# Performance work log

Hardware: AMD Instinct MI355X
Metric: run time of the kernel (lower is better)

The kernel has to match this reference:

```python
import jax, jax.numpy as jnp
import numpy as np

H = 56; W = 56; WS = 7; SHIFT = 3; C = 256; NH = 8
HD = C // NH; N = WS * WS; NW = (H // WS) * (W // WS)
SCALE = HD ** -0.5
LN_EPS = 1e-5


def _rel_pos_index():
    coords = np.stack(np.meshgrid(np.arange(WS), np.arange(WS), indexing='ij'))  # (2, ws, ws)
    cf = coords.reshape(2, -1)
    rel = (cf[:, :, None] - cf[:, None, :]).transpose(1, 2, 0)  # (N, N, 2)
    rel[..., 0] += WS - 1
    rel[..., 1] += WS - 1
    rel[..., 0] *= 2 * WS - 1
    return rel.sum(-1)  # (N, N) indices into (2*ws-1)^2 table

RPI = jnp.asarray(_rel_pos_index())


def _attn_mask():
    img = np.zeros((H, W))
    slices = (slice(0, -WS), slice(-WS, -SHIFT), slice(-SHIFT, None))
    cnt = 0
    for hs in slices:
        for ws_ in slices:
            img[hs, ws_] = cnt
            cnt += 1
    mw = img.reshape(H // WS, WS, W // WS, WS).transpose(0, 2, 1, 3).reshape(-1, N)
    diff = mw[:, None, :] - mw[:, :, None]  # (nW, N, N), [w,i,j] = mw[w,j]-mw[w,i]
    return jnp.asarray(np.where(diff != 0, -100.0, 0.0).astype(np.float32))

AMASK = _attn_mask()  # (nW, N, N)


def ln(x, g, b):
    m = x.mean(-1, keepdims=True)
    v = x.var(-1, keepdims=True)
    return (x - m) / jnp.sqrt(v + LN_EPS) * g + b


def win_part(x):  # (B, H, W, C) -> (B*nW, N, C)
    B = x.shape[0]
    return x.reshape(B, H // WS, WS, W // WS, WS, C).transpose(0, 1, 3, 2, 4, 5).reshape(-1, N, C)


def win_rev(xw, B):  # (B*nW, N, C) -> (B, H, W, C)
    return xw.reshape(B, H // WS, W // WS, WS, WS, C).transpose(0, 1, 3, 2, 4, 5).reshape(B, H, W, C)


def setup_inputs() -> dict:
    key = jax.random.key(0)
    ks = iter(jax.random.split(key, 40))
    B, L = 16, H * W
    Ch = int(C * 4.0)
    p = {}
    p['x'] = jax.random.normal(next(ks), (B, L, C), jnp.float32)
    p['x_SAR'] = jax.random.normal(next(ks), (B, L, C), jnp.float32)
    p['ln1_g'] = jnp.ones((C,)); p['ln1_b'] = jnp.zeros((C,))
    p['ln1s_g'] = jnp.ones((C,)); p['ln1s_b'] = jnp.zeros((C,))
    p['qkv_w'] = jax.random.normal(next(ks), (3 * C, C)) * 0.02
    p['qkv_b'] = jnp.zeros((3 * C,))
    p['qkvs_w'] = jax.random.normal(next(ks), (3 * C, C)) * 0.02
    p['qkvs_b'] = jnp.zeros((3 * C,))
    p['rpb_table'] = jax.random.normal(next(ks), ((2 * WS - 1) ** 2, NH)) * 0.02
    p['fuse_w'] = jax.random.normal(next(ks), (NH, NH)) * 0.1  # Conv2d(8,8,1) weight squeezed
    p['fuse_b'] = jnp.zeros((NH,))
    p['proj_w'] = jax.random.normal(next(ks), (C, C)) * 0.02
    p['proj_b'] = jnp.zeros((C,))
    p['projs_w'] = jax.random.normal(next(ks), (C, C)) * 0.02
    p['projs_b'] = jnp.zeros((C,))
    p['ln2_g'] = jnp.ones((C,)); p['ln2_b'] = jnp.zeros((C,))
    p['ln2s_g'] = jnp.ones((C,)); p['ln2s_b'] = jnp.zeros((C,))
    p['fc1_w'] = jax.random.normal(next(ks), (Ch, C)) * 0.02
    p['fc1_b'] = jnp.zeros((Ch,))
    p['fc2_w'] = jax.random.normal(next(ks), (C, Ch)) * 0.02
    p['fc2_b'] = jnp.zeros((C,))
    p['fc1s_w'] = jax.random.normal(next(ks), (Ch, C)) * 0.02
    p['fc1s_b'] = jnp.zeros((Ch,))
    p['fc2s_w'] = jax.random.normal(next(ks), (C, Ch)) * 0.02
    p['fc2s_b'] = jnp.zeros((C,))
    return p


def reference(x, x_SAR, ln1_g, ln1_b, ln1s_g, ln1s_b, qkv_w, qkv_b, qkvs_w, qkvs_b,
              rpb_table, fuse_w, fuse_b, proj_w, proj_b, projs_w, projs_b,
              ln2_g, ln2_b, ln2s_g, ln2s_b, fc1_w, fc1_b, fc2_w, fc2_b,
              fc1s_w, fc1s_b, fc2s_w, fc2s_b):
    B = x.shape[0]
    sc, sc_s = x, x_SAR

    def pre(xx, g, b):  # norm -> spatial -> cyclic shift -> windows
        xs = ln(xx, g, b).reshape(B, H, W, C)
        xs = jnp.roll(xs, (-SHIFT, -SHIFT), axis=(1, 2))
        return win_part(xs)

    xw = pre(x, ln1_g, ln1_b)
    xws = pre(x_SAR, ln1s_g, ln1s_b)

    def qkv_f(xin, Wt, bt):
        qkv = (xin @ Wt.T + bt).reshape(-1, N, 3, NH, HD).transpose(2, 0, 3, 1, 4)
        return qkv[0], qkv[1], qkv[2]  # each (B*nW, nH, N, HD)

    q, k, v = qkv_f(xw, qkv_w, qkv_b)
    qs, ks_, vs = qkv_f(xws, qkvs_w, qkvs_b)

    attn = jnp.einsum('bhnd,bhmd->bhnm', q * SCALE, k)
    attn_s = jnp.einsum('bhnd,bhmd->bhnm', qs * SCALE, ks_)

    rpb = rpb_table[RPI.reshape(-1)].reshape(N, N, NH).transpose(2, 0, 1)  # (nH, N, N)
    attn = attn + rpb[None]
    attn_s = attn_s + rpb[None]

    # shift-window mask add
    attn = (attn.reshape(B, NW, NH, N, N) + AMASK[None, :, None]).reshape(-1, NH, N, N)
    attn_s = (attn_s.reshape(B, NW, NH, N, N) + AMASK[None, :, None]).reshape(-1, NH, N, N)

    # dual-branch fusion: 1x1 conv over head dim + sigmoid gate
    diff = attn_s - attn
    gate = jax.nn.sigmoid(jnp.einsum('oh,bhnm->bonm', fuse_w, diff) + fuse_b[None, :, None, None])
    attn_f = jax.nn.softmax(attn + diff * gate, axis=-1)
    attn_s = jax.nn.softmax(attn_s, axis=-1)

    def out_f(a, vv, pw, pb):
        o = jnp.einsum('bhnm,bhmd->bhnd', a, vv).transpose(0, 2, 1, 3).reshape(-1, N, C)
        return o @ pw.T + pb

    xo = out_f(attn_f, v, proj_w, proj_b)
    xos = out_f(attn_s, vs, projs_w, projs_b)

    def post(xout, scc, g2, b2, w1, b1, w2, b2m):
        xr = jnp.roll(win_rev(xout, B), (SHIFT, SHIFT), axis=(1, 2)).reshape(B, -1, C)
        xr = scc + xr
        h = jax.nn.gelu(ln(xr, g2, b2) @ w1.T + b1, approximate=False)
        return xr + (h @ w2.T + b2m)

    out = post(xo, sc, ln2_g, ln2_b, fc1_w, fc1_b, fc2_w, fc2_b)
    out_s = post(xos, sc_s, ln2s_g, ln2s_b, fc1s_w, fc1s_b, fc2s_w, fc2s_b)
    return out, out_s
```

## Files before the change

kernel.cpp:

```cpp
#include <hip/hip_runtime.h>
#include <hip/hip_bf16.h>
#include <cstdio>

typedef unsigned short ushort_t;
using bf16x8  = __attribute__((ext_vector_type(8))) __bf16;
using u16x8   = __attribute__((ext_vector_type(8))) unsigned short;
using floatx4 = __attribute__((ext_vector_type(4))) float;

constexpr int    kTokens = 50176;
constexpr size_t TCsz    = (size_t)kTokens * 256;
constexpr float  kScale  = 0.17677669529663687f;
constexpr int    PSTR    = 904;
constexpr size_t VTP     = 2048;
constexpr size_t VTSZ    = (size_t)8192 * VTP;

__device__ __forceinline__ float bf2f(ushort_t u) {
  unsigned int x = (unsigned int)u << 16;
  return __uint_as_float(x);
}
__device__ __forceinline__ ushort_t f2bf(float f) {
  __hip_bfloat16 h = __float2bfloat16(f);
  return *(ushort_t*)&h;
}

__device__ __forceinline__ void gl_lds16(const ushort_t* g, ushort_t* l) {
  __builtin_amdgcn_global_load_lds(
      (const __attribute__((address_space(1))) unsigned int*)g,
      (__attribute__((address_space(3))) unsigned int*)l, 16, 0, 0);
}

__global__ __launch_bounds__(256) void f2b_k(const float* __restrict__ src,
                                             ushort_t* __restrict__ dst, int n) {
  int i = blockIdx.x * 256 + threadIdx.x;
  if (i < n) dst[i] = f2bf(src[i]);
}

__global__ __launch_bounds__(64) void bias2_k(const float* __restrict__ rpb,
                                              float* __restrict__ biasf) {
  const int b = blockIdx.x;
  const int head = b & 7, chunk = (b >> 3) & 3, cls = b >> 5;
  const int wh7 = cls >> 1, ww7 = cls & 1;
  const int lane = threadIdx.x;
  float* bp = biasf + ((size_t)b * 64 + lane) * 16;
#pragma unroll
  for (int nt = 0; nt < 4; ++nt) {
#pragma unroll
    for (int r = 0; r < 4; ++r) {
      const int row = chunk * 16 + (lane >> 4) * 4 + r;
      const int col = nt * 16 + (lane & 15);
      float val = 0.0f;
      if (row < 49 && col < 49) {
        const int yi = row / 7, xi = row % 7, yj = col / 7, xj = col % 7;
        val = rpb[((yi - yj + 6) * 13 + (xi - xj + 6)) * 8 + head];
        const int li = (wh7 ? (yi < 4 ? 1 : 2) : 0) * 3 + (ww7 ? (xi < 4 ? 1 : 2) : 0);
        const int lj = (wh7 ? (yj < 4 ? 1 : 2) : 0) * 3 + (ww7 ? (xj < 4 ? 1 : 2) : 0);
        if (li != lj) val -= 100.0f;
      }
      bp[nt * 4 + r] = val;
    }
  }
}

__global__ __launch_bounds__(256) void vtz_k(ushort_t* __restrict__ vtA,
                                             ushort_t* __restrict__ vtB) {
  const int id = blockIdx.x * 256 + threadIdx.x;
  ushort_t* base = (id < 262144) ? vtA : vtB;
  const size_t r = (size_t)(id & 262143) * 64;
  const uint4 z{0, 0, 0, 0};
  *(uint4*)(base + r + 48) = z;
  *(uint4*)(base + r + 56) = z;
}

template <int SHIFTED>
__global__ __launch_bounds__(256) void ln_k(const float* __restrict__ x,
                                            const float* __restrict__ g,
                                            const float* __restrict__ b,
                                            ushort_t* __restrict__ yout) {
  const int wave = threadIdx.x >> 6, lane = threadIdx.x & 63;
  const int t = blockIdx.x * 4 + wave;
  size_t src;
  if (SHIFTED) {
    int bb = t / 3136, r = t % 3136;
    int wi = r / 49, n = r % 49;
    int hp = (wi >> 3) * 7 + n / 7;
    int wp = (wi & 7) * 7 + n % 7;
    int sh = hp + 3; if (sh >= 56) sh -= 56;
    int sw = wp + 3; if (sw >= 56) sw -= 56;
    src = ((size_t)bb * 3136 + sh * 56 + sw) * 256;
  } else {
    src = (size_t)t * 256;
  }
  const float4 v4 = *(const float4*)(x + src + lane * 4);
  float s  = v4.x + v4.y + v4.z + v4.w;
  float s2 = v4.x * v4.x + v4.y * v4.y + v4.z * v4.z + v4.w * v4.w;
#pragma unroll
  for (int off = 32; off > 0; off >>= 1) {
    s  += __shfl_xor(s,  off);
    s2 += __shfl_xor(s2, off);
  }
  const float mean = s * (1.0f / 256.0f);
  const float var  = s2 * (1.0f / 256.0f) - mean * mean;
  const float rstd = rsqrtf(var + 1e-5f);
  const float4 g4 = *(const float4*)(g + lane * 4);
  const float4 b4 = *(const float4*)(b + lane * 4);
  ushort4 o;
  o.x = f2bf((v4.x - mean) * rstd * g4.x + b4.x);
  o.y = f2bf((v4.y - mean) * rstd * g4.y + b4.y);
  o.z = f2bf((v4.z - mean) * rstd * g4.z + b4.z);
  o.w = f2bf((v4.w - mean) * rstd * g4.w + b4.w);
  *(ushort4*)(yout + (size_t)t * 256 + lane * 4) = o;
}

template <int MODE>
__global__ __launch_bounds__(256) void bgemm_k(const ushort_t* __restrict__ A,
                                               const ushort_t* __restrict__ W,
                                               const float* __restrict__ bias,
                                               float* __restrict__ outf,
                                               ushort_t* __restrict__ outb,
                                               const float* __restrict__ aux,
                                               int K, int Nc) {
  __shared__ __align__(16) ushort_t As[2 * 4096];
  __shared__ __align__(16) ushort_t Bs[2 * 4096];
  const int tid = threadIdx.x;
  const int nbx = gridDim.x;
  const int nwg = nbx * gridDim.y;
  int flat = blockIdx.y * nbx + blockIdx.x;
  {
    const int xcd = flat & 7, idx = flat >> 3;
    const int q8 = nwg >> 3, r8 = nwg & 7;
    flat = (xcd < r8 ? xcd * (q8 + 1) : r8 * (q8 + 1) + (xcd - r8) * q8) + idx;
  }
  const int m0 = (flat / nbx) * 128;
  const int n0 = (flat % nbx) * 128;
  const int lane = tid & 63, wv = tid >> 6;
  const int wm = (wv >> 1) * 64, wn = (wv & 1) * 64;
  const int l16 = lane & 15, quad = lane >> 4;

  const int srow = tid >> 2;
  const int gkc  = (tid & 3) ^ ((tid >> 3) & 3);
  const ushort_t* Ag0 = A + (size_t)(m0 + srow) * K + gkc * 8;
  const ushort_t* Ag1 = A + (size_t)(m0 + 64 + srow) * K + gkc * 8;
  const ushort_t* Wg0 = W + (size_t)(n0 + srow) * K + gkc * 8;
  const ushort_t* Wg1 = W + (size_t)(n0 + 64 + srow) * K + gkc * 8;
  const int ldsW0 = wv * 512, ldsW1 = 2048 + wv * 512;

  const int kcq = quad ^ ((l16 >> 1) & 3);
  const int arA = (wm + l16) * 32 + kcq * 8;
  const int arB = (wn + l16) * 32 + kcq * 8;

  const int NT = K >> 5;
  floatx4 acc[4][4] = {};

  gl_lds16(Ag0, As + ldsW0);
  gl_lds16(Ag1, As + ldsW1);
  gl_lds16(Wg0, Bs + ldsW0);
  gl_lds16(Wg1, Bs + ldsW1);
  __syncthreads();

  int cur = 0;
  for (int t = 0; t < NT; ++t) {
    if (t + 1 < NT) {
      const int k0 = (t + 1) * 32;
      const int nb = (cur ^ 1) * 4096;
      gl_lds16(Ag0 + k0, As + nb + ldsW0);
      gl_lds16(Ag1 + k0, As + nb + ldsW1);
      gl_lds16(Wg0 + k0, Bs + nb + ldsW0);
      gl_lds16(Wg1 + k0, Bs + nb + ldsW1);
    }
    const int cb = cur * 4096;
    bf16x8 af[4], bfr[4];
#pragma unroll
    for (int tt = 0; tt < 4; ++tt) {
      af[tt]  = *(const bf16x8*)&As[cb + arA + tt * 512];
      bfr[tt] = *(const bf16x8*)&Bs[cb + arB + tt * 512];
    }
#pragma unroll
    for (int mt = 0; mt < 4; ++mt)
#pragma unroll
      for (int nt = 0; nt < 4; ++nt)
        acc[mt][nt] = __builtin_amdgcn_mfma_f32_16x16x32_bf16(af[mt], bfr[nt], acc[mt][nt], 0, 0, 0);
    __syncthreads();
    cur ^= 1;
  }

  if (MODE == 0) {
    int wis[16], ns[16];
#pragma unroll
    for (int mt = 0; mt < 4; ++mt) {
      int row = m0 + wm + mt * 16 + quad * 4;
      int wi = row / 49, n = row - wi * 49;
#pragma unroll
      for (int r = 0; r < 4; ++r) {
        wis[mt * 4 + r] = wi; ns[mt * 4 + r] = n;
        if (++n == 49) { n = 0; ++wi; }
      }
    }
    if (n0 < 512) {
      size_t rb[16];
#pragma unroll
      for (int i = 0; i < 16; ++i) rb[i] = (size_t)wis[i] * 12544 + (size_t)ns[i] * 32;
#pragma unroll
      for (int nt = 0; nt < 4; ++nt) {
        const int col = n0 + wn + nt * 16 + l16;
        const int which = col >> 8, head = (col >> 5) & 7, d = col & 31;
        const float bv = bias[col];
        const float sc = (which == 0) ? kScale : 1.0f;
        ushort_t* ob = outb + (size_t)which * TCsz + head * 1568 + d;
#pragma unroll
        for (int i = 0; i < 16; ++i)
          ob[rb[i]] = f2bf((acc[i >> 2][nt][i & 3] + bv) * sc);
      }
    } else {
      size_t rb[16];
#pragma unroll
      for (int i = 0; i < 16; ++i) rb[i] = (size_t)wis[i] * 16384 + (size_t)ns[i];
      ushort_t* vtb = (ushort_t*)outf;
#pragma unroll
      for (int nt = 0; nt < 4; ++nt) {
        const int col = n0 + wn + nt * 16 + l16;
        const int head = (col >> 5) & 7, d = col & 31;
        const float bv = bias[col];
        ushort_t* ob = vtb + head * 2048 + d * 64;
#pragma unroll
        for (int i = 0; i < 16; ++i)
          ob[rb[i]] = f2bf(acc[i >> 2][nt][i & 3] + bv);
      }
    }
  } else if (MODE == 1) {
    size_t rb[16];
#pragma unroll
    for (int mt = 0; mt < 4; ++mt) {
#pragma unroll
      for (int r = 0; r < 4; ++r) {
        const int row = m0 + wm + mt * 16 + quad * 4 + r;
        const int wi = row / 49, n = row - wi * 49;
        const int b = wi >> 6, wl = wi & 63;
        int h = (wl >> 3) * 7 + n / 7 + 3; if (h >= 56) h -= 56;
        int w = (wl & 7) * 7 + n % 7 + 3; if (w >= 56) w -= 56;
        rb[mt * 4 + r] = ((size_t)(b * 3136 + h * 56 + w)) * 256;
      }
    }
#pragma unroll
    for (int nt = 0; nt < 4; ++nt) {
      const int col = n0 + wn + nt * 16 + l16;
      const float bv = bias[col];
#pragma unroll
      for (int i = 0; i < 16; ++i) {
        const size_t idx = rb[i] + col;
        outf[idx] = aux[idx] + acc[i >> 2][nt][i & 3] + bv;
      }
    }
  } else if (MODE == 2) {
    size_t rb[16];
#pragma unroll
    for (int mt = 0; mt < 4; ++mt)
#pragma unroll
      for (int r = 0; r < 4; ++r)
        rb[mt * 4 + r] = (size_t)(m0 + wm + mt * 16 + quad * 4 + r) * Nc;
#pragma unroll
    for (int nt = 0; nt < 4; ++nt) {
      const int col = n0 + wn + nt * 16 + l16;
      const float bv = bias[col];
#pragma unroll
      for (int i = 0; i < 16; ++i) {
        float val = acc[i >> 2][nt][i & 3] + bv;
        val = 0.5f * val * (1.0f + erff(val * 0.70710678118654752f));
        outb[rb[i] + col] = f2bf(val);
      }
    }
  } else {
    size_t rb[16];
#pragma unroll
    for (int mt = 0; mt < 4; ++mt)
#pragma unroll
      for (int r = 0; r < 4; ++r)
        rb[mt * 4 + r] = (size_t)(m0 + wm + mt * 16 + quad * 4 + r) * 256;
#pragma unroll
    for (int nt = 0; nt < 4; ++nt) {
      const int col = n0 + wn + nt * 16 + l16;
      const float bv = bias[col];
#pragma unroll
      for (int i = 0; i < 16; ++i) {
        const size_t idx = rb[i] + col;
        outf[idx] = aux[idx] + acc[i >> 2][nt][i & 3] + bv;
      }
    }
  }
}

__global__ __launch_bounds__(256) void attn_k(const ushort_t* __restrict__ qA,
                                              const ushort_t* __restrict__ qB,
                                              const ushort_t* __restrict__ vtA,
                                              const ushort_t* __restrict__ vtB,
                                              const float* __restrict__ biasf,
                                              const float* __restrict__ fw,
                                              const float* __restrict__ fb,
                                              ushort_t* __restrict__ Obase) {
  __shared__ __align__(16) ushort_t S[16 * PSTR];
  __shared__ float fwl[64], fbl[8];
  __shared__ float linv[256];
  const int tid = threadIdx.x, lane = tid & 63, wv = tid >> 6;
  const int l16 = lane & 15, quad = lane >> 4;
  int bx = blockIdx.x;
  bx = (bx & 7) * 512 + (bx >> 3);
  const int win = bx >> 2, chunk = bx & 3;
  const int r0 = chunk * 16;
  const int rows = (r0 + 16 <= 49) ? 16 : (49 - r0);

  if (rows < 16) {
    const int per = (16 - rows) * 7;
    for (int u = tid; u < 16 * per; u += 256) {
      const int pr = u / per, off = u - pr * per;
      *(uint4*)(S + pr * PSTR + rows * 56 + off * 8) = uint4{0, 0, 0, 0};
    }
  }
  if (tid < 16) *(uint4*)(S + tid * PSTR + 896) = uint4{0, 0, 0, 0};
  if (tid < 64) fwl[tid] = fw[tid];
  if (tid < 8)  fbl[tid] = fb[tid];
  __syncthreads();

  const int wl = win & 63;
  const int cls = (((wl >> 3) == 7) ? 2 : 0) + (((wl & 7) == 7) ? 1 : 0);

  const int qrow = (r0 + l16 <= 48) ? (r0 + l16) : 48;
#pragma unroll
  for (int i = 0; i < 4; ++i) {
    const int pair = wv * 4 + i;
    const int br = pair >> 3, h = pair & 7;
    const ushort_t* qb = (br ? qB : qA) + (size_t)(win * 8 + h) * 1568;
    const ushort_t* kb = qb + TCsz;
    const bf16x8 af = *(const bf16x8*)(qb + qrow * 32 + quad * 8);
    floatx4 acc[4];
#pragma unroll
    for (int nt = 0; nt < 4; ++nt) {
      const int krow = nt * 16 + l16;
      const int krc = (krow <= 48) ? krow : 48;
      const bf16x8 bfr = *(const bf16x8*)(kb + krc * 32 + quad * 8);
      acc[nt] = __builtin_amdgcn_mfma_f32_16x16x32_bf16(af, bfr, (floatx4){0.f, 0.f, 0.f, 0.f}, 0, 0, 0);
    }
    const float* bfp = biasf + ((size_t)((cls * 4 + chunk) * 8 + h) * 64 + lane) * 16;
    ushort_t* Sp = S + pair * PSTR;
#pragma unroll
    for (int nt = 0; nt < 4; ++nt) {
      const int col = nt * 16 + l16;
      if (col >= 56) continue;
      const float4 bv4 = *(const float4*)(bfp + nt * 4);
      const float bvv[4] = {bv4.x, bv4.y, bv4.z, bv4.w};
#pragma unroll
      for (int r = 0; r < 4; ++r) {
        const int lrow = quad * 4 + r;
        if (lrow < rows)
          Sp[lrow * 56 + col] = (col < 49) ? f2bf(acc[nt][r] + bvv[r]) : (ushort_t)0;
      }
    }
  }
  __syncthreads();

  const int np = rows * 49;
  for (int p = tid; p < np; p += 256) {
    const int lr = p / 49, c = p - lr * 49;
    const int off = lr * 56 + c;
    float sA[8], dd[8];
#pragma unroll
    for (int h = 0; h < 8; ++h) {
      sA[h] = bf2f(S[h * PSTR + off]);
      dd[h] = bf2f(S[(8 + h) * PSTR + off]) - sA[h];
    }
#pragma unroll
    for (int o = 0; o < 8; ++o) {
      float g = fbl[o];
#pragma unroll
      for (int h = 0; h < 8; ++h) g = fmaf(fwl[o * 8 + h], dd[h], g);
      g = __builtin_amdgcn_rcpf(1.0f + __expf(-g));
      S[o * PSTR + off] = f2bf(sA[o] + dd[o] * g);
    }
  }
  __syncthreads();

  {
    const int lr = tid & 15, ph = tid >> 4;
    if (lr < rows) {
      ushort_t* row = S + ph * PSTR + lr * 56;
      bf16x8 c[7];
#pragma unroll
      for (int j = 0; j < 7; ++j) c[j] = *(const bf16x8*)(row + j * 8);
      float mx = -1e30f;
#pragma unroll
      for (int j = 0; j < 6; ++j)
#pragma unroll
        for (int e = 0; e < 8; ++e) mx = fmaxf(mx, (float)c[j][e]);
      mx = fmaxf(mx, (float)c[6][0]);
      float sum = 0.0f;
#pragma unroll
      for (int j = 0; j < 6; ++j) {
        u16x8 o;
#pragma unroll
        for (int e = 0; e < 8; ++e) {
          const float ev = __expf((float)c[j][e] - mx);
          sum += ev;
          o[e] = f2bf(ev);
        }
        *(u16x8*)(row + j * 8) = o;
      }
      {
        const float ev = __expf((float)c[6][0] - mx);
        sum += ev;
        u16x8 o = {};
        o[0] = f2bf(ev);
        *(u16x8*)(row + 48) = o;
      }
      linv[tid] = __builtin_amdgcn_rcpf(sum);
    } else {
      linv[tid] = 1.0f;
    }
  }
  __syncthreads();

#pragma unroll
  for (int i = 0; i < 4; ++i) {
    const int pair = wv * 4 + i;
    const int br = pair >> 3, h = pair & 7;
    const ushort_t* vt = (br ? vtB : vtA) + (size_t)(win * 8 + h) * VTP;
    const ushort_t* Sp = S + pair * PSTR;
    floatx4 acc[2] = {};
#pragma unroll
    for (int ks = 0; ks < 2; ++ks) {
      const bf16x8 af = *(const bf16x8*)(Sp + l16 * 56 + ks * 32 + quad * 8);
#pragma unroll
      for (int nt = 0; nt < 2; ++nt) {
        const bf16x8 bv = *(const bf16x8*)(vt + (nt * 16 + l16) * 64 + ks * 32 + quad * 8);
        acc[nt] = __builtin_amdgcn_mfma_f32_16x16x32_bf16(af, bv, acc[nt], 0, 0, 0);
      }
    }
    ushort_t* Ob = Obase + (size_t)br * TCsz + (size_t)(win * 49 + r0) * 256 + h * 32;
#pragma unroll
    for (int nt = 0; nt < 2; ++nt)
#pragma unroll
      for (int r = 0; r < 4; ++r) {
        const int n = quad * 4 + r;
        if (n < rows)
          Ob[(size_t)n * 256 + nt * 16 + l16] = f2bf(acc[nt][r] * linv[pair * 16 + n]);
      }
  }
}

extern "C" void kernel_launch(void* const* d_in, const int* in_sizes, int n_in,
                              void* d_out, int out_size, void* d_ws, size_t ws_size,
                              hipStream_t stream) {
  if (n_in < 29) { fprintf(stderr, "kernel_launch: expected 29 inputs, got %d\n", n_in); return; }
  const float* x      = (const float*)d_in[0];
  const float* xsar   = (const float*)d_in[1];
  const float* ln1_g  = (const float*)d_in[2];
  const float* ln1_b  = (const float*)d_in[3];
  const float* ln1s_g = (const float*)d_in[4];
  const float* ln1s_b = (const float*)d_in[5];
  const float* qkv_w  = (const float*)d_in[6];
  const float* qkv_b  = (const float*)d_in[7];
  const float* qkvs_w = (const float*)d_in[8];
  const float* qkvs_b = (const float*)d_in[9];
  const float* rpb    = (const float*)d_in[10];
  const float* fuse_w = (const float*)d_in[11];
  const float* fuse_b = (const float*)d_in[12];
  const float* proj_w = (const float*)d_in[13];
  const float* proj_b = (const float*)d_in[14];
  const float* projs_w = (const float*)d_in[15];
  const float* projs_b = (const float*)d_in[16];
  const float* ln2_g  = (const float*)d_in[17];
  const float* ln2_b  = (const float*)d_in[18];
  const float* ln2s_g = (const float*)d_in[19];
  const float* ln2s_b = (const float*)d_in[20];
  const float* fc1_w  = (const float*)d_in[21];
  const float* fc1_b  = (const float*)d_in[22];
  const float* fc2_w  = (const float*)d_in[23];
  const float* fc2_b  = (const float*)d_in[24];
  const float* fc1s_w = (const float*)d_in[25];
  const float* fc1s_b = (const float*)d_in[26];
  const float* fc2s_w = (const float*)d_in[27];
  const float* fc2s_b = (const float*)d_in[28];
  float* out = (float*)d_out;
  float* ws  = (float*)d_ws;

  const size_t need = 8 * TCsz * sizeof(float);
  if (ws_size < need) {
    fprintf(stderr, "kernel_launch: ws_size %zu < needed %zu\n", ws_size, need);
    return;
  }

  ushort_t* H   = (ushort_t*)ws;
  ushort_t* xw  = H;
  ushort_t* xws = H + TCsz;
  ushort_t* q   = H + 2 * TCsz;
  ushort_t* qs  = H + 5 * TCsz;
  ushort_t* vtA = H + 8 * TCsz;
  ushort_t* vtB = vtA + VTSZ;
  float* xr  = ws + 6 * TCsz;
  float* xrs = ws + 7 * TCsz;
  ushort_t* y   = H + 2 * TCsz;
  ushort_t* ysb = H + 3 * TCsz;
  ushort_t* hbuf = H + 4 * TCsz;
  ushort_t* wb  = H + 12 * TCsz - 1572864;
  float* biasf = (float*)(H + 12 * TCsz - 1572864 - 262144);
  ushort_t* wqkv  = wb;
  ushort_t* wqkvs = wb + 196608;
  ushort_t* wproj = wb + 393216;
  ushort_t* wprojs= wb + 458752;
  ushort_t* wfc1  = wb + 524288;
  ushort_t* wfc1s = wb + 786432;
  ushort_t* wfc2  = wb + 1048576;
  ushort_t* wfc2s = wb + 1310720;

  f2b_k<<<768, 256, 0, stream>>>(qkv_w,  wqkv,  196608);
  f2b_k<<<768, 256, 0, stream>>>(qkvs_w, wqkvs, 196608);
  f2b_k<<<256, 256, 0, stream>>>(proj_w, wproj, 65536);
  f2b_k<<<256, 256, 0, stream>>>(projs_w,wprojs,65536);
  f2b_k<<<1024,256, 0, stream>>>(fc1_w,  wfc1,  262144);
  f2b_k<<<1024,256, 0, stream>>>(fc1s_w, wfc1s, 262144);
  f2b_k<<<1024,256, 0, stream>>>(fc2_w,  wfc2,  262144);
  f2b_k<<<1024,256, 0, stream>>>(fc2s_w, wfc2s, 262144);
  bias2_k<<<128, 64, 0, stream>>>(rpb, biasf);
  vtz_k<<<2048, 256, 0, stream>>>(vtA, vtB);

  ln_k<1><<<12544, 256, 0, stream>>>(x,    ln1_g,  ln1_b,  xw);
  ln_k<1><<<12544, 256, 0, stream>>>(xsar, ln1s_g, ln1s_b, xws);
  bgemm_k<0><<<dim3(6, 392), 256, 0, stream>>>(xw,  wqkv,  qkv_b,  (float*)vtA, q,  nullptr, 256, 768);
  bgemm_k<0><<<dim3(6, 392), 256, 0, stream>>>(xws, wqkvs, qkvs_b, (float*)vtB, qs, nullptr, 256, 768);
  attn_k<<<4096, 256, 0, stream>>>(q, qs, vtA, vtB, biasf, fuse_w, fuse_b, H);
  bgemm_k<1><<<dim3(2, 392), 256, 0, stream>>>(H,        wproj,  proj_b,  xr,  nullptr, x,    256, 256);
  bgemm_k<1><<<dim3(2, 392), 256, 0, stream>>>(H + TCsz, wprojs, projs_b, xrs, nullptr, xsar, 256, 256);
  ln_k<0><<<12544, 256, 0, stream>>>(xr,  ln2_g,  ln2_b,  y);
  ln_k<0><<<12544, 256, 0, stream>>>(xrs, ln2s_g, ln2s_b, ysb);
  bgemm_k<2><<<dim3(8, 392), 256, 0, stream>>>(y,    wfc1,  fc1_b,  nullptr, hbuf, nullptr, 256, 1024);
  bgemm_k<3><<<dim3(2, 392), 256, 0, stream>>>(hbuf, wfc2,  fc2_b,  out,     nullptr, xr,  1024, 256);
  bgemm_k<2><<<dim3(8, 392), 256, 0, stream>>>(ysb,  wfc1s, fc1s_b, nullptr, hbuf, nullptr, 256, 1024);
  bgemm_k<3><<<dim3(2, 392), 256, 0, stream>>>(hbuf, wfc2s, fc2s_b, out + TCsz, nullptr, xrs, 1024, 256);
}
```

Measured before the change: 928.8 us.

## Register-stage GEMM tile loads and prefetch attention Q/K/V operands early

The GEMM mainloop swaps direct global-to-LDS loads for register-staged loads into a double-buffered LDS pipeline. Loads for two tiles ahead are issued before each compute step, with explicit waitcnt and barriers placed around sched_barrier. The attention kernel also issues its Q, K and V global loads into registers earlier, so they overlap the LDS zeroing, the gate and the softmax phases. This raises register pressure and can lower occupancy, and the hand-written waitcnt encoding must be correct for the target.

Result: faster. 909.3 us (-2.1%).

```diff
diff --git a/kernel.cpp b/kernel.cpp
--- a/kernel.cpp
+++ b/kernel.cpp
@@ -21,12 +21,6 @@
 __device__ __forceinline__ ushort_t f2bf(float f) {
   __hip_bfloat16 h = __float2bfloat16(f);
   return *(ushort_t*)&h;
-}
-
-__device__ __forceinline__ void gl_lds16(const ushort_t* g, ushort_t* l) {
-  __builtin_amdgcn_global_load_lds(
-      (const __attribute__((address_space(1))) unsigned int*)g,
-      (__attribute__((address_space(3))) unsigned int*)l, 16, 0, 0);
 }
 
 __global__ __launch_bounds__(256) void f2b_k(const float* __restrict__ src,
@@ -142,7 +136,8 @@
   const ushort_t* Ag1 = A + (size_t)(m0 + 64 + srow) * K + gkc * 8;
   const ushort_t* Wg0 = W + (size_t)(n0 + srow) * K + gkc * 8;
   const ushort_t* Wg1 = W + (size_t)(n0 + 64 + srow) * K + gkc * 8;
-  const int ldsW0 = wv * 512, ldsW1 = 2048 + wv * 512;
+  const int w0 = wv * 512 + lane * 8;
+  const int w1 = 2048 + wv * 512 + lane * 8;
 
   const int kcq = quad ^ ((l16 >> 1) & 3);
   const int arA = (wm + l16) * 32 + kcq * 8;
@@ -150,38 +145,43 @@
 
   const int NT = K >> 5;
   floatx4 acc[4][4] = {};
-
-  gl_lds16(Ag0, As + ldsW0);
-  gl_lds16(Ag1, As + ldsW1);
-  gl_lds16(Wg0, Bs + ldsW0);
-  gl_lds16(Wg1, Bs + ldsW1);
-  __syncthreads();
-
-  int cur = 0;
-  for (int t = 0; t < NT; ++t) {
-    if (t + 1 < NT) {
-      const int k0 = (t + 1) * 32;
-      const int nb = (cur ^ 1) * 4096;
-      gl_lds16(Ag0 + k0, As + nb + ldsW0);
-      gl_lds16(Ag1 + k0, As + nb + ldsW1);
-      gl_lds16(Wg0 + k0, Bs + nb + ldsW0);
-      gl_lds16(Wg1 + k0, Bs + nb + ldsW1);
-    }
-    const int cb = cur * 4096;
-    bf16x8 af[4], bfr[4];
-#pragma unroll
-    for (int tt = 0; tt < 4; ++tt) {
-      af[tt]  = *(const bf16x8*)&As[cb + arA + tt * 512];
-      bfr[tt] = *(const bf16x8*)&Bs[cb + arB + tt * 512];
-    }
-#pragma unroll
-    for (int mt = 0; mt < 4; ++mt)
-#pragma unroll
-      for (int nt = 0; nt < 4; ++nt)
-        acc[mt][nt] = __builtin_amdgcn_mfma_f32_16x16x32_bf16(af[mt], bfr[nt], acc[mt][nt], 0, 0, 0);
-    __syncthreads();
-    cur ^= 1;
-  }
+  uint4 pa0, pa1, pb0, pb1, qa0, qa1, qb0, qb1;
+
+#define BG_LOAD(r0, r1, r2, r3, k0) { r0 = *(const uint4*)(Ag0 + (k0)); \
+    r1 = *(const uint4*)(Ag1 + (k0)); r2 = *(const uint4*)(Wg0 + (k0)); \
+    r3 = *(const uint4*)(Wg1 + (k0)); }
+#define BG_WRITE(r0, r1, r2, r3, cb) { *(uint4*)&As[(cb) + w0] = r0; \
+    *(uint4*)&As[(cb) + w1] = r1; *(uint4*)&Bs[(cb) + w0] = r2; \
+    *(uint4*)&Bs[(cb) + w1] = r3; }
+#define BG_BAR() { __builtin_amdgcn_sched_barrier(0); \
+    __builtin_amdgcn_s_waitcnt(0xC07F);  \
+    __builtin_amdgcn_s_barrier(); __builtin_amdgcn_sched_barrier(0); }
+#define BG_COMP(cb) { bf16x8 af[4], bfr[4]; \
+    _Pragma("unroll") for (int tt = 0; tt < 4; ++tt) { \
+      af[tt]  = *(const bf16x8*)&As[(cb) + arA + tt * 512]; \
+      bfr[tt] = *(const bf16x8*)&Bs[(cb) + arB + tt * 512]; } \
+    _Pragma("unroll") for (int mt = 0; mt < 4; ++mt) \
+    _Pragma("unroll") for (int nt = 0; nt < 4; ++nt) \
+      acc[mt][nt] = __builtin_amdgcn_mfma_f32_16x16x32_bf16(af[mt], bfr[nt], acc[mt][nt], 0, 0, 0); }
+
+  BG_LOAD(pa0, pa1, pb0, pb1, 0);
+  BG_WRITE(pa0, pa1, pb0, pb1, 0);
+  BG_LOAD(qa0, qa1, qb0, qb1, 32);
+  BG_BAR();
+  for (int t = 0; t < NT; t += 2) {
+    if (t + 2 < NT) BG_LOAD(pa0, pa1, pb0, pb1, (t + 2) * 32);
+    BG_WRITE(qa0, qa1, qb0, qb1, 4096);
+    BG_COMP(0);
+    BG_BAR();
+    if (t + 3 < NT) BG_LOAD(qa0, qa1, qb0, qb1, (t + 3) * 32);
+    if (t + 2 < NT) BG_WRITE(pa0, pa1, pb0, pb1, 0);
+    BG_COMP(4096);
+    BG_BAR();
+  }
+#undef BG_LOAD
+#undef BG_WRITE
+#undef BG_BAR
+#undef BG_COMP
 
   if (MODE == 0) {
     int wis[16], ns[16];
@@ -307,6 +307,23 @@
   const int r0 = chunk * 16;
   const int rows = (r0 + 16 <= 49) ? 16 : (49 - r0);
 
+  const int qrow = (r0 + l16 <= 48) ? (r0 + l16) : 48;
+  bf16x8 afq[4], bk[4][4];
+#pragma unroll
+  for (int i = 0; i < 4; ++i) {
+    const int pair = wv * 4 + i;
+    const int br = pair >> 3, h = pair & 7;
+    const ushort_t* qb = (br ? qB : qA) + (size_t)(win * 8 + h) * 1568;
+    const ushort_t* kb = qb + TCsz;
+    afq[i] = *(const bf16x8*)(qb + qrow * 32 + quad * 8);
+#pragma unroll
+    for (int nt = 0; nt < 4; ++nt) {
+      const int krow = nt * 16 + l16;
+      const int krc = (krow <= 48) ? krow : 48;
+      bk[i][nt] = *(const bf16x8*)(kb + krc * 32 + quad * 8);
+    }
+  }
+
   if (rows < 16) {
     const int per = (16 - rows) * 7;
     for (int u = tid; u < 16 * per; u += 256) {
@@ -322,30 +339,24 @@
   const int wl = win & 63;
   const int cls = (((wl >> 3) == 7) ? 2 : 0) + (((wl & 7) == 7) ? 1 : 0);
 
-  const int qrow = (r0 + l16 <= 48) ? (r0 + l16) : 48;
 #pragma unroll
   for (int i = 0; i < 4; ++i) {
     const int pair = wv * 4 + i;
-    const int br = pair >> 3, h = pair & 7;
-    const ushort_t* qb = (br ? qB : qA) + (size_t)(win * 8 + h) * 1568;
-    const ushort_t* kb = qb + TCsz;
-    const bf16x8 af = *(const bf16x8*)(qb + qrow * 32 + quad * 8);
+    const int h = pair & 7;
+    const float* bfp = biasf + ((size_t)((cls * 4 + chunk) * 8 + h) * 64 + lane) * 16;
+    float4 bv4[4];
+#pragma unroll
+    for (int nt = 0; nt < 4; ++nt) bv4[nt] = *(const float4*)(bfp + nt * 4);
     floatx4 acc[4];
 #pragma unroll
-    for (int nt = 0; nt < 4; ++nt) {
-      const int krow = nt * 16 + l16;
-      const int krc = (krow <= 48) ? krow : 48;
-      const bf16x8 bfr = *(const bf16x8*)(kb + krc * 32 + quad * 8);
-      acc[nt] = __builtin_amdgcn_mfma_f32_16x16x32_bf16(af, bfr, (floatx4){0.f, 0.f, 0.f, 0.f}, 0, 0, 0);
-    }
-    const float* bfp = biasf + ((size_t)((cls * 4 + chunk) * 8 + h) * 64 + lane) * 16;
+    for (int nt = 0; nt < 4; ++nt)
+      acc[nt] = __builtin_amdgcn_mfma_f32_16x16x32_bf16(afq[i], bk[i][nt], (floatx4){0.f, 0.f, 0.f, 0.f}, 0, 0, 0);
     ushort_t* Sp = S + pair * PSTR;
 #pragma unroll
     for (int nt = 0; nt < 4; ++nt) {
       const int col = nt * 16 + l16;
       if (col >= 56) continue;
-      const float4 bv4 = *(const float4*)(bfp + nt * 4);
-      const float bvv[4] = {bv4.x, bv4.y, bv4.z, bv4.w};
+      const float bvv[4] = {bv4[nt].x, bv4[nt].y, bv4[nt].z, bv4[nt].w};
 #pragma unroll
       for (int r = 0; r < 4; ++r) {
         const int lrow = quad * 4 + r;
@@ -355,6 +366,19 @@
     }
   }
   __syncthreads();
+
+  bf16x8 vf[4][4];
+#pragma unroll
+  for (int i = 0; i < 4; ++i) {
+    const int pair = wv * 4 + i;
+    const int br = pair >> 3, h = pair & 7;
+    const ushort_t* vt = (br ? vtB : vtA) + (size_t)(win * 8 + h) * VTP;
+#pragma unroll
+    for (int nt = 0; nt < 2; ++nt)
+#pragma unroll
+      for (int ks = 0; ks < 2; ++ks)
+        vf[i][nt * 2 + ks] = *(const bf16x8*)(vt + (nt * 16 + l16) * 64 + ks * 32 + quad * 8);
+  }
 
   const int np = rows * 49;
   for (int p = tid; p < np; p += 256) {
@@ -420,17 +444,14 @@
   for (int i = 0; i < 4; ++i) {
     const int pair = wv * 4 + i;
     const int br = pair >> 3, h = pair & 7;
-    const ushort_t* vt = (br ? vtB : vtA) + (size_t)(win * 8 + h) * VTP;
     const ushort_t* Sp = S + pair * PSTR;
     floatx4 acc[2] = {};
 #pragma unroll
     for (int ks = 0; ks < 2; ++ks) {
       const bf16x8 af = *(const bf16x8*)(Sp + l16 * 56 + ks * 32 + quad * 8);
 #pragma unroll
-      for (int nt = 0; nt < 2; ++nt) {
-        const bf16x8 bv = *(const bf16x8*)(vt + (nt * 16 + l16) * 64 + ks * 32 + quad * 8);
-        acc[nt] = __builtin_amdgcn_mfma_f32_16x16x32_bf16(af, bv, acc[nt], 0, 0, 0);
-      }
+      for (int nt = 0; nt < 2; ++nt)
+        acc[nt] = __builtin_amdgcn_mfma_f32_16x16x32_bf16(af, vf[i][nt * 2 + ks], acc[nt], 0, 0, 0);
     }
     ushort_t* Ob = Obase + (size_t)br * TCsz + (size_t)(win * 49 + r0) * 256 + h * 32;
 #pragma unroll
```
